# Kernel tuning notes

Measured on AMD Instinct MI355X. Metric: run time of the kernel, lower is better.

## Reference

```python
import jax, jax.numpy as jnp
import numpy as np

TAU = 2.0      # LIF membrane time constant
ALPHA = 2.0    # ATan surrogate alpha (spikingjelly default)
EPS = 1e-5     # BatchNorm eps

@jax.custom_vjp
def atan_spike(x):
    # Heaviside forward, ATan surrogate backward (spikingjelly surrogate.ATan)
    return (x >= 0.0).astype(x.dtype)

def _atan_fwd(x):
    return atan_spike(x), x

def _atan_bwd(x, g):
    return (g * (ALPHA / 2.0) / (1.0 + (jnp.pi / 2.0 * ALPHA * x) ** 2),)

atan_spike.defvjp(_atan_fwd, _atan_bwd)


def setup_inputs() -> dict:
    key = jax.random.key(0)
    ks = jax.random.split(key, 3)
    B, T, F, O = 32, 512, 64, 64  # batch, window_size, num_raw_features, output_size
    inputs = jax.random.normal(ks[0], (B, T, F), jnp.float32)
    enc_w = jax.random.normal(ks[1], (O, 1), jnp.float32) * 0.5   # nn.Linear(1, O) weight
    enc_b = jax.random.normal(ks[2], (O,), jnp.float32) * 0.1     # bias
    bn_w = jnp.ones((1,), jnp.float32)      # BatchNorm2d(1) affine weight
    bn_b = jnp.zeros((1,), jnp.float32)     # affine bias
    bn_mean = jnp.zeros((1,), jnp.float32)  # running mean (eval mode)
    bn_var = jnp.ones((1,), jnp.float32)    # running var (eval mode)
    return {"inputs": inputs, "enc_w": enc_w, "enc_b": enc_b,
            "bn_w": bn_w, "bn_b": bn_b, "bn_mean": bn_mean, "bn_var": bn_var}


def reference(inputs, enc_w, enc_b, bn_w, bn_b, bn_mean, bn_var):
    # temporal diff: delta[:,0]=0, delta[:,t]=x[:,t]-x[:,t-1]   [B,T,F]
    delta = jnp.concatenate(
        [jnp.zeros_like(inputs[:, :1]), inputs[:, 1:] - inputs[:, :-1]], axis=1)
    x = jnp.transpose(delta[:, None], (0, 1, 3, 2))  # [B,1,F,T]
    # BatchNorm2d(1), eval mode (single channel)
    inv = bn_w[None, :, None, None] * jax.lax.rsqrt(bn_var[None, :, None, None] + EPS)
    x = (x - bn_mean[None, :, None, None]) * inv + bn_b[None, :, None, None]
    x = jnp.transpose(x, (0, 2, 3, 1))                # [B,F,T,1]
    enc = x * enc_w[:, 0] + enc_b                     # Linear(1,O): [B,F,T,O]
    enc = jnp.transpose(enc, (3, 0, 1, 2))            # [O,B,F,T]; scan over leading axis O

    def step(v, xt):
        h = v + (xt - v) / TAU                         # neuronal charge (decay_input, v_reset=0)
        s = atan_spike(h - 1.0)                        # fire at v_threshold=1
        v_next = (1.0 - jax.lax.stop_gradient(s)) * h  # hard reset to 0, detach_reset=True
        return v_next, s

    v0 = jnp.zeros(enc.shape[1:], enc.dtype)
    _, spks = jax.lax.scan(step, v0, enc)             # [O,B,F,T]
    return jnp.transpose(spks, (1, 0, 2, 3))          # [B,O,F,T]
```

## Files before the change

kernel.cpp:

```cpp
#include <hip/hip_runtime.h>
#include <math.h>


#define B_DIM 32
#define T_DIM 512
#define F_DIM 64
#define O_DIM 64

typedef float v4f __attribute__((ext_vector_type(4)));

__global__ __launch_bounds__(1024) void delta_lif_kernel(
    const float* __restrict__ in,
    const float* __restrict__ enc_w,
    const float* __restrict__ enc_b,
    const float* __restrict__ bn_w,
    const float* __restrict__ bn_b,
    const float* __restrict__ bn_mean,
    const float* __restrict__ bn_var,
    float* __restrict__ out)
{
#pragma clang fp contract(off)
    const float vpe  = bn_var[0] + 1e-5f;
    const float r    = (float)(1.0 / sqrt((double)vpe));
    const float inv  = bn_w[0] * r;
    const float mean = bn_mean[0];
    const float bnb  = bn_b[0];

    const int b  = blockIdx.x;
    const int lt = threadIdx.x;
    const int fsub = lt >> 7;
    const int t0   = (lt & 127) << 2;

    for (int oct = 0; oct < 8; ++oct) {
        const int f = (oct << 3) + fsub;

        const float* pin = in + b * (T_DIM * F_DIM) + f;
        const float c0 = pin[(t0 + 0) * F_DIM];
        const float c1 = pin[(t0 + 1) * F_DIM];
        const float c2 = pin[(t0 + 2) * F_DIM];
        const float c3 = pin[(t0 + 3) * F_DIM];
        const float p  = (t0 == 0) ? c0 : pin[(t0 - 1) * F_DIM];

        const float x0 = ((c0 - p)  - mean) * inv + bnb;
        const float x1 = ((c1 - c0) - mean) * inv + bnb;
        const float x2 = ((c2 - c1) - mean) * inv + bnb;
        const float x3 = ((c3 - c2) - mean) * inv + bnb;

        float v0 = 0.0f, v1 = 0.0f, v2 = 0.0f, v3 = 0.0f;

        float* pout = out + (b << 21) + (f << 9) + t0;

#pragma unroll 8
        for (int o = 0; o < O_DIM; ++o) {
            const float w  = enc_w[o];
            const float bb = enc_b[o];

            const float e0 = x0 * w + bb;
            const float e1 = x1 * w + bb;
            const float e2 = x2 * w + bb;
            const float e3 = x3 * w + bb;

            const float h0 = v0 + (e0 - v0) * 0.5f;
            const float h1 = v1 + (e1 - v1) * 0.5f;
            const float h2 = v2 + (e2 - v2) * 0.5f;
            const float h3 = v3 + (e3 - v3) * 0.5f;

            const bool g0 = (h0 >= 1.0f);
            const bool g1 = (h1 >= 1.0f);
            const bool g2 = (h2 >= 1.0f);
            const bool g3 = (h3 >= 1.0f);

            v4f s;
            s.x = g0 ? 1.0f : 0.0f;
            s.y = g1 ? 1.0f : 0.0f;
            s.z = g2 ? 1.0f : 0.0f;
            s.w = g3 ? 1.0f : 0.0f;

            v0 = g0 ? 0.0f : h0;
            v1 = g1 ? 0.0f : h1;
            v2 = g2 ? 0.0f : h2;
            v3 = g3 ? 0.0f : h3;

            *(v4f*)(pout + (o << 15)) = s;
        }
    }
}

extern "C" void kernel_launch(void* const* d_in, const int* in_sizes, int n_in,
                              void* d_out, int out_size, void* d_ws, size_t ws_size,
                              hipStream_t stream) {
    const float* in      = (const float*)d_in[0];
    const float* enc_w   = (const float*)d_in[1];
    const float* enc_b   = (const float*)d_in[2];
    const float* bn_w    = (const float*)d_in[3];
    const float* bn_b    = (const float*)d_in[4];
    const float* bn_mean = (const float*)d_in[5];
    const float* bn_var  = (const float*)d_in[6];
    float* out = (float*)d_out;

    delta_lif_kernel<<<dim3(32), dim3(1024), 0, stream>>>(
        in, enc_w, enc_b, bn_w, bn_b, bn_mean, bn_var, out);
}
```

Measured before the change: 333.3 us.

## Split output-channel scan across blocks with recomputed prefix to fill all CUs

The grid grows from 32 blocks (one per batch) to 256 blocks. Each block now handles one batch and one eighth of the output-channel scan, and reaches the right membrane state by recomputing the earlier channels without writing them. Each thread now keeps all 8 feature groups in registers. Block indices are remapped so that neighbouring blocks cover different batches. This fixes the underuse of a 256-CU device at the cost of redundant prefix arithmetic (up to 7x extra on the last slice) and higher register pressure.

After: 309.3 us. -7.2%, faster.

```diff
diff --git a/kernel.cpp b/kernel.cpp
--- a/kernel.cpp
+++ b/kernel.cpp
@@ -9,7 +9,7 @@
 
 typedef float v4f __attribute__((ext_vector_type(4)));
 
-__global__ __launch_bounds__(1024) void delta_lif_kernel(
+__global__ __launch_bounds__(1024, 4) void delta_lif_kernel(
     const float* __restrict__ in,
     const float* __restrict__ enc_w,
     const float* __restrict__ enc_b,
@@ -26,62 +26,70 @@
     const float mean = bn_mean[0];
     const float bnb  = bn_b[0];
 
-    const int b  = blockIdx.x;
+    const int bid  = blockIdx.x;
+    const int vbid = ((bid & 7) << 5) + (bid >> 3);
+    const int b    = vbid >> 3;
+    const int oe   = vbid & 7;
+
     const int lt = threadIdx.x;
     const int fsub = lt >> 7;
     const int t0   = (lt & 127) << 2;
 
-    for (int oct = 0; oct < 8; ++oct) {
-        const int f = (oct << 3) + fsub;
+    float x[8][4];
+    float v[8][4];
 
+#pragma unroll
+    for (int j = 0; j < 8; ++j) {
+        const int f = (j << 3) + fsub;
         const float* pin = in + b * (T_DIM * F_DIM) + f;
         const float c0 = pin[(t0 + 0) * F_DIM];
         const float c1 = pin[(t0 + 1) * F_DIM];
         const float c2 = pin[(t0 + 2) * F_DIM];
         const float c3 = pin[(t0 + 3) * F_DIM];
         const float p  = (t0 == 0) ? c0 : pin[(t0 - 1) * F_DIM];
+        x[j][0] = ((c0 - p)  - mean) * inv + bnb;
+        x[j][1] = ((c1 - c0) - mean) * inv + bnb;
+        x[j][2] = ((c2 - c1) - mean) * inv + bnb;
+        x[j][3] = ((c3 - c2) - mean) * inv + bnb;
+        v[j][0] = 0.0f; v[j][1] = 0.0f; v[j][2] = 0.0f; v[j][3] = 0.0f;
+    }
 
-        const float x0 = ((c0 - p)  - mean) * inv + bnb;
-        const float x1 = ((c1 - c0) - mean) * inv + bnb;
-        const float x2 = ((c2 - c1) - mean) * inv + bnb;
-        const float x3 = ((c3 - c2) - mean) * inv + bnb;
+    const int o_begin = oe << 3;
 
-        float v0 = 0.0f, v1 = 0.0f, v2 = 0.0f, v3 = 0.0f;
+    for (int o = 0; o < o_begin; ++o) {
+        const float w  = enc_w[o];
+        const float bb = enc_b[o];
+#pragma unroll
+        for (int j = 0; j < 8; ++j) {
+#pragma unroll
+            for (int k = 0; k < 4; ++k) {
+                const float e = x[j][k] * w + bb;
+                const float h = v[j][k] + (e - v[j][k]) * 0.5f;
+                v[j][k] = (h >= 1.0f) ? 0.0f : h;
+            }
+        }
+    }
 
-        float* pout = out + (b << 21) + (f << 9) + t0;
+    float* pbase = out + (b << 21) + (lt << 2);
 
-#pragma unroll 8
-        for (int o = 0; o < O_DIM; ++o) {
-            const float w  = enc_w[o];
-            const float bb = enc_b[o];
-
-            const float e0 = x0 * w + bb;
-            const float e1 = x1 * w + bb;
-            const float e2 = x2 * w + bb;
-            const float e3 = x3 * w + bb;
-
-            const float h0 = v0 + (e0 - v0) * 0.5f;
-            const float h1 = v1 + (e1 - v1) * 0.5f;
-            const float h2 = v2 + (e2 - v2) * 0.5f;
-            const float h3 = v3 + (e3 - v3) * 0.5f;
-
-            const bool g0 = (h0 >= 1.0f);
-            const bool g1 = (h1 >= 1.0f);
-            const bool g2 = (h2 >= 1.0f);
-            const bool g3 = (h3 >= 1.0f);
-
+#pragma unroll
+    for (int oi = 0; oi < 8; ++oi) {
+        const int o = o_begin + oi;
+        const float w  = enc_w[o];
+        const float bb = enc_b[o];
+        float* pplane = pbase + (o << 15);
+#pragma unroll
+        for (int j = 0; j < 8; ++j) {
             v4f s;
-            s.x = g0 ? 1.0f : 0.0f;
-            s.y = g1 ? 1.0f : 0.0f;
-            s.z = g2 ? 1.0f : 0.0f;
-            s.w = g3 ? 1.0f : 0.0f;
-
-            v0 = g0 ? 0.0f : h0;
-            v1 = g1 ? 0.0f : h1;
-            v2 = g2 ? 0.0f : h2;
-            v3 = g3 ? 0.0f : h3;
-
-            *(v4f*)(pout + (o << 15)) = s;
+#pragma unroll
+            for (int k = 0; k < 4; ++k) {
+                const float e = x[j][k] * w + bb;
+                const float h = v[j][k] + (e - v[j][k]) * 0.5f;
+                const bool g = (h >= 1.0f);
+                ((float*)&s)[k] = g ? 1.0f : 0.0f;
+                v[j][k] = g ? 0.0f : h;
+            }
+            *(v4f*)(pplane + (j << 12)) = s;
         }
     }
 }
@@ -98,6 +106,6 @@
     const float* bn_var  = (const float*)d_in[6];
     float* out = (float*)d_out;
 
-    delta_lif_kernel<<<dim3(32), dim3(1024), 0, stream>>>(
+    delta_lif_kernel<<<dim3(256), dim3(1024), 0, stream>>>(
         in, enc_w, enc_b, bn_w, bn_b, bn_mean, bn_var, out);
 }
```
